# Kernel optimization log

Hardware: AMD Instinct MI355X
Metric: run time of the kernel (lower is better)

The kernel has to match this reference:

```python
import jax, jax.numpy as jnp
import numpy as np

M = 256
N = 256
J = 2
L = 4
F = J * L  # number of Morlet wavelets
PI = float(np.pi)


def _make_grid(m, n):
    gm = np.arange(-(m // 2), -(m // 2) + m, dtype=np.float32)
    gn = np.arange(-(n // 2), -(n // 2) + n, dtype=np.float32)
    return jnp.asarray(np.stack(np.meshgrid(gm, gn, indexing='ij'), 0))  # [2, M, N]

GRID = _make_grid(M, N)


def morlet_filters(theta, xis, sigmas, slants, morlet=True):
    """Build Fourier-domain Morlet (or Gabor/Gaussian) filters, [F, M, N] complex64."""
    c, s = jnp.cos(theta), jnp.sin(theta)
    wave_vectors = jnp.stack([c, s], axis=1) * xis[:, None]                   # [F, 2]
    # orthonormal basis per filter: row0 along wave direction, row1 perpendicular
    basis = jnp.stack([jnp.stack([c, s], 1), jnp.stack([-s, c], 1)], axis=1)  # [F, 2, 2]
    gauss_dirs = basis / sigmas[:, None, None]
    slant_mod = jnp.stack([slants, jnp.ones_like(slants)], axis=1)            # [F, 2]
    gauss_dirs = gauss_dirs * slant_mod[:, :, None]
    phase = jnp.einsum('fd,dmn->fmn', wave_vectors, GRID)                     # [F, M, N]
    waves = jnp.exp(1j * phase)
    radii2 = jnp.sum(jnp.einsum('fed,dmn->femn', gauss_dirs, GRID) ** 2, axis=1)
    gauss = jnp.exp(-0.5 * radii2)
    if morlet:
        gs = gauss.sum(axis=(-2, -1), keepdims=True)
        ws = (waves * gauss).sum(axis=(-2, -1), keepdims=True)
        filt = (waves - ws / gs) * gauss  # zero-mean Morlet correction
    else:
        filt = waves * gauss
    norm = (2.0 * PI * sigmas * sigmas / slants)[:, None, None]
    filt = filt / norm
    filt = jnp.fft.ifftshift(filt, axes=(-2, -1))
    return jnp.fft.fft2(filt)


def low_pass_phi():
    # Gaussian low-pass at scale 2**J (xi = 0, Gabor without Morlet correction)
    th = jnp.zeros((1,), jnp.float32)
    xi = jnp.zeros((1,), jnp.float32)
    sg = jnp.full((1,), 0.8 * 2.0 ** J, jnp.float32)
    sl = jnp.ones((1,), jnp.float32)
    return morlet_filters(th, xi, sg, sl, morlet=False)[0]  # [M, N]


def setup_inputs() -> dict:
    key = jax.random.key(0)
    x = jax.random.normal(key, (4, 2, M, N), dtype=jnp.float32)
    # Tight-Frame initialization of the J*L learnable wavelet parameters
    js = np.repeat(np.arange(J), L).astype(np.float32)
    theta = np.tile((int(L - L / 2 - 1) - np.arange(L)) * np.pi / L, J).astype(np.float32)
    xis = (3.0 / 4.0 * np.pi / 2.0 ** js).astype(np.float32)
    sigmas = (0.8 * 2.0 ** js).astype(np.float32)
    slants = np.full(J * L, 4.0 / L, dtype=np.float32)
    return {"x": x, "theta": jnp.asarray(theta), "xis": jnp.asarray(xis),
            "sigmas": jnp.asarray(sigmas), "slants": jnp.asarray(slants)}


def reference(x, theta, xis, sigmas, slants):
    """Order-2 wavelet scattering on periodic fields via FFT conv + modulus.
    Returns [B, (1 + F + F*F) * C, M, N]."""
    B, C = x.shape[0], x.shape[1]
    sub = 1  # subsample factor (module default)
    psi = morlet_filters(theta, xis, sigmas, slants)        # [F, M, N] complex
    phi = low_pass_phi()                                    # [M, N] complex
    Xh = jnp.fft.fft2(x)                                    # [B, C, M, N]
    S0 = jnp.fft.ifft2(Xh * phi).real[:, :, None]           # [B, C, 1, M, N]
    U1 = jnp.abs(jnp.fft.ifft2(Xh[:, :, None] * psi))       # [B, C, F, M, N]
    U1h = jnp.fft.fft2(U1)
    U2 = jnp.abs(jnp.fft.ifft2(U1h[:, :, :, None] * psi))   # [B, C, F, F, M, N]
    S = jnp.concatenate([S0, U1, U2.reshape(B, C, F * F, M, N)], axis=2)
    S = S[..., ::sub, ::sub]
    return S.reshape(B, (1 + F + F * F) * C, M // sub, N // sub)
```

## Files before the change

kernel.cpp:

```cpp
#include <hip/hip_runtime.h>
#include <math.h>

#define PI_F 3.14159265358979323846f
#define IMG 65536

__device__ __forceinline__ float2 cmul(float2 a, float2 b) {
  return make_float2(a.x * b.x - a.y * b.y, a.x * b.y + a.y * b.x);
}
__device__ __forceinline__ float2 shflx(float2 v, int m) {
  return make_float2(__shfl_xor(v.x, m, 64), __shfl_xor(v.y, m, 64));
}


__device__ __forceinline__ void fft64_dif(float2 v[4], int lane) {
  #pragma unroll
  for (int st = 5; st >= 0; --st) {
    int s = 1 << st;
    float ang = -PI_F * (float)(lane & (s - 1)) / (float)s;
    float sn, cs; __sincosf(ang, &sn, &cs);
    bool hi = (lane & s) != 0;
    #pragma unroll
    for (int r = 0; r < 4; ++r) {
      float2 p = shflx(v[r], s);
      if (hi) {
        float2 d = make_float2(p.x - v[r].x, p.y - v[r].y);
        v[r] = make_float2(d.x * cs - d.y * sn, d.x * sn + d.y * cs);
      } else {
        v[r] = make_float2(v[r].x + p.x, v[r].y + p.y);
      }
    }
  }
}

__device__ __forceinline__ void fft64_dit(float2 v[4], int lane) {
  #pragma unroll
  for (int st = 0; st <= 5; ++st) {
    int s = 1 << st;
    float ang = PI_F * (float)(lane & (s - 1)) / (float)s;
    float sn, cs; __sincosf(ang, &sn, &cs);
    bool hi = (lane & s) != 0;
    #pragma unroll
    for (int r = 0; r < 4; ++r) {
      float2 p = shflx(v[r], s);
      if (hi) {
        float2 wb = make_float2(v[r].x * cs - v[r].y * sn, v[r].x * sn + v[r].y * cs);
        v[r] = make_float2(p.x - wb.x, p.y - wb.y);
      } else {
        float2 wb = make_float2(p.x * cs - p.y * sn, p.x * sn + p.y * cs);
        v[r] = make_float2(v[r].x + wb.x, v[r].y + wb.y);
      }
    }
  }
}

__device__ __forceinline__ void fwd256(float2 v[4], int lane) {
  float2 e0 = make_float2(v[0].x + v[2].x, v[0].y + v[2].y);
  float2 o0 = make_float2(v[0].x - v[2].x, v[0].y - v[2].y);
  float2 e1 = make_float2(v[1].x + v[3].x, v[1].y + v[3].y);
  float2 o1 = make_float2(v[1].x - v[3].x, v[1].y - v[3].y);
  v[0] = make_float2(e0.x + e1.x, e0.y + e1.y);
  v[2] = make_float2(e0.x - e1.x, e0.y - e1.y);
  v[1] = make_float2(o0.x + o1.y, o0.y - o1.x);
  v[3] = make_float2(o0.x - o1.y, o0.y + o1.x);
  float sn, cs; __sincosf(2.f * PI_F * (float)lane * (1.f / 256.f), &sn, &cs);
  float2 w1 = make_float2(cs, -sn);
  float2 w2 = cmul(w1, w1);
  float2 w3 = cmul(w2, w1);
  v[1] = cmul(v[1], w1); v[2] = cmul(v[2], w2); v[3] = cmul(v[3], w3);
  fft64_dif(v, lane);
}

__device__ __forceinline__ void inv256(float2 v[4], int lane) {
  fft64_dit(v, lane);
  float sn, cs; __sincosf(2.f * PI_F * (float)lane * (1.f / 256.f), &sn, &cs);
  float2 w1 = make_float2(cs, sn);
  float2 w2 = cmul(w1, w1);
  float2 w3 = cmul(w2, w1);
  v[1] = cmul(v[1], w1); v[2] = cmul(v[2], w2); v[3] = cmul(v[3], w3);
  float2 e0 = make_float2(v[0].x + v[2].x, v[0].y + v[2].y);
  float2 o0 = make_float2(v[0].x - v[2].x, v[0].y - v[2].y);
  float2 e1 = make_float2(v[1].x + v[3].x, v[1].y + v[3].y);
  float2 o1 = make_float2(v[1].x - v[3].x, v[1].y - v[3].y);
  v[0] = make_float2(e0.x + e1.x, e0.y + e1.y);
  v[2] = make_float2(e0.x - e1.x, e0.y - e1.y);
  v[1] = make_float2(o0.x - o1.y, o0.y + o1.x);
  v[3] = make_float2(o0.x + o1.y, o0.y - o1.x);
}

__device__ __forceinline__ void tile_flush(float2 (*tile)[258], float2* OT, int r0) {
  __syncthreads();
  int t = threadIdx.x;
  float4* dst = (float4*)(OT + (size_t)t * 256 + r0);
  #pragma unroll
  for (int k = 0; k < 4; ++k) {
    float2 a = tile[2 * k][t], b = tile[2 * k + 1][t];
    dst[k] = make_float4(a.x, a.y, b.x, b.y);
  }
}


__global__ __launch_bounds__(256) void k_sums(const float* th, const float* xi,
                                              const float* sg, const float* sl,
                                              float* sums) {
  int f = blockIdx.x, t = threadIdx.x;
  float c, s;
  sincosf(th[f], &s, &c);
  float X = xi[f], S = sg[f], SL = sl[f];
  float a0x = SL * c / S, a0y = SL * s / S, a1x = -s / S, a1y = c / S;
  float gs = 0.f, wr = 0.f, wi = 0.f;
  for (int p = t; p < IMG; p += 256) {
    float gm = (float)((p >> 8) - 128);
    float gn = (float)((p & 255) - 128);
    float r0 = a0x * gm + a0y * gn, r1 = a1x * gm + a1y * gn;
    float g = __expf(-0.5f * (r0 * r0 + r1 * r1));
    float sp, cp;
    sincosf(X * (c * gm + s * gn), &sp, &cp);
    gs += g; wr += cp * g; wi += sp * g;
  }
  __shared__ float red[3][256];
  red[0][t] = gs; red[1][t] = wr; red[2][t] = wi;
  __syncthreads();
  for (int o = 128; o > 0; o >>= 1) {
    if (t < o) {
      red[0][t] += red[0][t + o];
      red[1][t] += red[1][t + o];
      red[2][t] += red[2][t + o];
    }
    __syncthreads();
  }
  if (t == 0) {
    sums[f * 3 + 0] = red[0][0];
    sums[f * 3 + 1] = red[1][0];
    sums[f * 3 + 2] = red[2][0];
  }
}

__global__ __launch_bounds__(256) void k_spatial(const float* th, const float* xi,
                                                 const float* sg, const float* sl,
                                                 const float* sums, float2* spat) {
  int f = blockIdx.y;
  int p = blockIdx.x * 256 + threadIdx.x;
  int m = p >> 8, n = p & 255;
  float gm = (m < 128) ? (float)m : (float)(m - 256);
  float gn = (n < 128) ? (float)n : (float)(n - 256);
  bool isPhi = (f == 8);
  float T = isPhi ? 0.f : th[f];
  float X = isPhi ? 0.f : xi[f];
  float S = isPhi ? 3.2f : sg[f];
  float SL = isPhi ? 1.f : sl[f];
  float c, s;
  sincosf(T, &s, &c);
  float a0x = SL * c / S, a0y = SL * s / S, a1x = -s / S, a1y = c / S;
  float r0 = a0x * gm + a0y * gn, r1 = a1x * gm + a1y * gn;
  float g = __expf(-0.5f * (r0 * r0 + r1 * r1));
  float sp, cp;
  sincosf(X * (c * gm + s * gn), &sp, &cp);
  float re, im;
  if (!isPhi) {
    float gs = sums[f * 3];
    float Kr = sums[f * 3 + 1] / gs, Ki = sums[f * 3 + 2] / gs;
    re = (cp - Kr) * g;
    im = (sp - Ki) * g;
  } else {
    re = g;
    im = 0.f;
  }
  float inorm = SL / (2.f * PI_F * S * S);
  spat[(size_t)f * IMG + p] = make_float2(re * inorm, im * inorm);
}


__global__ __launch_bounds__(256) void k_fwdT(const float2* __restrict__ in,
                                              float2* __restrict__ out) {
  __shared__ float2 tile[8][258];
  int w = threadIdx.x >> 6, l = threadIdx.x & 63;
  int img = blockIdx.y, r0 = blockIdx.x * 8;
  const float2* ib = in + (size_t)img * IMG;
  #pragma unroll
  for (int it = 0; it < 2; ++it) {
    int ri = w + 4 * it;
    const float2* ip = ib + (size_t)(r0 + ri) * 256;
    float2 v[4];
    #pragma unroll
    for (int j = 0; j < 4; ++j) v[j] = ip[l + 64 * j];
    fwd256(v, l);
    #pragma unroll
    for (int j = 0; j < 4; ++j) tile[ri][l + 64 * j] = v[j];
  }
  tile_flush(tile, out + (size_t)img * IMG, r0);
}

__global__ __launch_bounds__(256) void k_fwdT_real(const float* __restrict__ in,
                                                   float2* __restrict__ out) {
  __shared__ float2 tile[8][258];
  int w = threadIdx.x >> 6, l = threadIdx.x & 63;
  int img = blockIdx.y, r0 = blockIdx.x * 8;
  const float* ib = in + (size_t)img * IMG;
  #pragma unroll
  for (int it = 0; it < 2; ++it) {
    int ri = w + 4 * it;
    const float* ip = ib + (size_t)(r0 + ri) * 256;
    float2 v[4];
    #pragma unroll
    for (int j = 0; j < 4; ++j) v[j] = make_float2(ip[l + 64 * j], 0.f);
    fwd256(v, l);
    #pragma unroll
    for (int j = 0; j < 4; ++j) tile[ri][l + 64 * j] = v[j];
  }
  tile_flush(tile, out + (size_t)img * IMG, r0);
}

__global__ __launch_bounds__(256) void k_fwdS(const float2* in, float2* out) {
  int w = threadIdx.x >> 6, l = threadIdx.x & 63;
  int img = blockIdx.y, row = blockIdx.x * 4 + w;
  const float2* ip = in + (size_t)img * IMG + (size_t)row * 256;
  float2 v[4];
  #pragma unroll
  for (int j = 0; j < 4; ++j) v[j] = ip[l + 64 * j];
  fwd256(v, l);
  float2* op = out + (size_t)img * IMG + (size_t)row * 256;
  #pragma unroll
  for (int j = 0; j < 4; ++j) op[l + 64 * j] = v[j];
}

__device__ __forceinline__ void mul_inv_tile(const float2* A, const float2* P,
                                             float2* OT, int r0, int w, int l,
                                             float2 (*tile)[258]) {
  #pragma unroll
  for (int it = 0; it < 2; ++it) {
    int ri = w + 4 * it;
    const float2* ap = A + (size_t)(r0 + ri) * 256;
    const float2* pp = P + (size_t)(r0 + ri) * 256;
    float2 v[4];
    #pragma unroll
    for (int j = 0; j < 4; ++j) v[j] = cmul(ap[l + 64 * j], pp[l + 64 * j]);
    inv256(v, l);
    #pragma unroll
    for (int j = 0; j < 4; ++j) tile[ri][l + 64 * j] = v[j];
  }
  tile_flush(tile, OT, r0);
}

__global__ __launch_bounds__(256) void k_s0_p1(const float2* __restrict__ XhT,
                                               const float2* __restrict__ phiT,
                                               float2* __restrict__ s0t) {
  __shared__ float2 tile[8][258];
  int w = threadIdx.x >> 6, l = threadIdx.x & 63;
  int img = blockIdx.y, r0 = blockIdx.x * 8;
  mul_inv_tile(XhT + (size_t)img * IMG, phiT, s0t + (size_t)img * IMG, r0, w, l, tile);
}

__global__ __launch_bounds__(256) void k_s0_p2(const float2* __restrict__ s0t,
                                               float* __restrict__ out) {
  int w = threadIdx.x >> 6, l = threadIdx.x & 63;
  int img = blockIdx.y, row = blockIdx.x * 4 + w;
  const float2* ip = s0t + (size_t)img * IMG + (size_t)row * 256;
  float2 v[4];
  #pragma unroll
  for (int j = 0; j < 4; ++j) v[j] = ip[l + 64 * j];
  inv256(v, l);
  float* op = out + ((size_t)img * 73) * IMG + (size_t)row * 256;
  #pragma unroll
  for (int j = 0; j < 4; ++j) op[l + 64 * j] = v[j].x * (1.f / 65536.f);
}

__global__ __launch_bounds__(256) void k_u1_p1(const float2* __restrict__ XhT,
                                               const float2* __restrict__ psiT,
                                               float* out) {
  __shared__ float2 tile[8][258];
  int w = threadIdx.x >> 6, l = threadIdx.x & 63;
  int u = blockIdx.y, i = u >> 3, f = u & 7;
  int r0 = blockIdx.x * 8;
  float2* t1 = (float2*)out + ((size_t)(i * 73 + 9 + 2 * f)) * 32768;
  mul_inv_tile(XhT + (size_t)i * IMG, psiT + (size_t)f * IMG, t1, r0, w, l, tile);
}

__global__ __launch_bounds__(256) void k_u1_p2(float* out, float2* T2) {
  __shared__ float2 tile[8][258];
  int w = threadIdx.x >> 6, l = threadIdx.x & 63;
  int u = blockIdx.y, i = u >> 3, f = u & 7;
  int r0 = blockIdx.x * 8;
  const float2* t1 = (const float2*)out + ((size_t)(i * 73 + 9 + 2 * f)) * 32768;
  float* uo = out + ((size_t)(i * 73 + 1 + f)) * IMG;
  #pragma unroll
  for (int it = 0; it < 2; ++it) {
    int ri = w + 4 * it, row = r0 + ri;
    const float2* ip = t1 + (size_t)row * 256;
    float2 v[4];
    #pragma unroll
    for (int j = 0; j < 4; ++j) v[j] = ip[l + 64 * j];
    inv256(v, l);
    float* up = uo + (size_t)row * 256;
    #pragma unroll
    for (int j = 0; j < 4; ++j) {
      float2 z = v[j];
      float mod = sqrtf(z.x * z.x + z.y * z.y) * (1.f / 65536.f);
      up[l + 64 * j] = mod;
      v[j] = make_float2(mod, 0.f);
    }
    fwd256(v, l);
    #pragma unroll
    for (int j = 0; j < 4; ++j) tile[ri][l + 64 * j] = v[j];
  }
  tile_flush(tile, T2 + (size_t)u * IMG, r0);
}

__global__ __launch_bounds__(256) void k_u2_p1(const float2* __restrict__ U1hT,
                                               const float2* __restrict__ psiT,
                                               float2* __restrict__ T3,
                                               int f1, int i0) {
  __shared__ float2 tile[8][258];
  int w = threadIdx.x >> 6, l = threadIdx.x & 63;
  int y = blockIdx.y, ii = i0 + (y >> 3), f2 = y & 7;
  int r0 = blockIdx.x * 8;
  mul_inv_tile(U1hT + ((size_t)(ii * 8 + f1)) * IMG, psiT + (size_t)f2 * IMG,
               T3 + (size_t)y * IMG, r0, w, l, tile);
}

__global__ __launch_bounds__(256) void k_u2_p2(const float2* __restrict__ T3,
                                               float* __restrict__ out,
                                               int f1, int i0) {
  int w = threadIdx.x >> 6, l = threadIdx.x & 63;
  int y = blockIdx.y, ii = i0 + (y >> 3), f2 = y & 7;
  int row = blockIdx.x * 4 + w;
  const float2* ip = T3 + (size_t)y * IMG + (size_t)row * 256;
  float2 v[4];
  #pragma unroll
  for (int j = 0; j < 4; ++j) v[j] = ip[l + 64 * j];
  inv256(v, l);
  float* op = out + ((size_t)(ii * 73 + 9 + f1 * 8 + f2)) * IMG + (size_t)row * 256;
  #pragma unroll
  for (int j = 0; j < 4; ++j) {
    float2 z = v[j];
    op[l + 64 * j] = sqrtf(z.x * z.x + z.y * z.y) * (1.f / 65536.f);
  }
}

extern "C" void kernel_launch(void* const* d_in, const int* in_sizes, int n_in,
                              void* d_out, int out_size, void* d_ws, size_t ws_size,
                              hipStream_t stream) {
  const float* x  = (const float*)d_in[0];
  const float* th = (const float*)d_in[1];
  const float* xi = (const float*)d_in[2];
  const float* sg = (const float*)d_in[3];
  const float* sl = (const float*)d_in[4];
  float* out = (float*)d_out;

  float* sums  = (float*)d_ws;
  float2* psiT = (float2*)((char*)d_ws + 1024);
  float2* XhT  = psiT + (size_t)9 * IMG;
  float2* T2   = XhT + (size_t)8 * IMG;
  float2* T3   = T2 + (size_t)64 * IMG;
  float2* spat = T2;
  float2* tmp9 = T2 + (size_t)9 * IMG;
  float2* xtmp = T2;
  float2* s0t  = T2;

  size_t t3off = 1024 + (size_t)(9 + 8 + 64) * IMG * sizeof(float2);
  int nI = 8;
  while (nI > 1 && t3off + (size_t)nI * 8 * IMG * sizeof(float2) > ws_size) nI >>= 1;

  dim3 B(256);
  k_sums<<<dim3(8), B, 0, stream>>>(th, xi, sg, sl, sums);
  k_spatial<<<dim3(256, 9), B, 0, stream>>>(th, xi, sg, sl, sums, spat);
  k_fwdT<<<dim3(32, 9), B, 0, stream>>>(spat, tmp9);
  k_fwdS<<<dim3(64, 9), B, 0, stream>>>(tmp9, psiT);
  k_fwdT_real<<<dim3(32, 8), B, 0, stream>>>(x, xtmp);
  k_fwdS<<<dim3(64, 8), B, 0, stream>>>(xtmp, XhT);
  k_s0_p1<<<dim3(32, 8), B, 0, stream>>>(XhT, psiT + (size_t)8 * IMG, s0t);
  k_s0_p2<<<dim3(64, 8), B, 0, stream>>>(s0t, out);
  k_u1_p1<<<dim3(32, 64), B, 0, stream>>>(XhT, psiT, out);
  k_u1_p2<<<dim3(32, 64), B, 0, stream>>>(out, T2);
  k_fwdS<<<dim3(64, 64), B, 0, stream>>>(T2, T2);
  for (int f1 = 0; f1 < 8; ++f1)
    for (int i0 = 0; i0 < 8; i0 += nI) {
      k_u2_p1<<<dim3(32, nI * 8), B, 0, stream>>>(T2, psiT, T3, f1, i0);
      k_u2_p2<<<dim3(64, nI * 8), B, 0, stream>>>(T3, out, f1, i0);
    }
}
```

Baseline: 581.1 us.

## Batch eight rows per wave in register FFTs with precomputed twiddles and fewer launches

Each wave now transforms 8 rows held in registers and writes the transpose straight to global memory with float4 stores, dropping the shared-memory tile and its barrier. Twiddles are computed once per lane in a struct and reused across all rows and both passes, replacing per-stage sincos calls. The spatial filter build is fused into the first FFT pass, S0 is folded into the U1 kernels as a ninth filter, and the U2 loop is batched into larger chunks so far fewer kernels are launched. The cost is much higher register pressure from 32 complex values per lane plus twiddles, which may lower occupancy, and the transposed stores are strided across columns.

Result: faster. 539.5 us (-7.2%).

```diff
diff --git a/kernel.cpp b/kernel.cpp
--- a/kernel.cpp
+++ b/kernel.cpp
@@ -11,90 +11,133 @@
   return make_float2(__shfl_xor(v.x, m, 64), __shfl_xor(v.y, m, 64));
 }
 
-
-__device__ __forceinline__ void fft64_dif(float2 v[4], int lane) {
-  #pragma unroll
-  for (int st = 5; st >= 0; --st) {
-    int s = 1 << st;
-    float ang = -PI_F * (float)(lane & (s - 1)) / (float)s;
-    float sn, cs; __sincosf(ang, &sn, &cs);
-    bool hi = (lane & s) != 0;
-    #pragma unroll
-    for (int r = 0; r < 4; ++r) {
-      float2 p = shflx(v[r], s);
-      if (hi) {
-        float2 d = make_float2(p.x - v[r].x, p.y - v[r].y);
-        v[r] = make_float2(d.x * cs - d.y * sn, d.x * sn + d.y * cs);
-      } else {
-        v[r] = make_float2(v[r].x + p.x, v[r].y + p.y);
+struct Tw { float2 w[5]; float2 q1, q2, q3; };
+
+__device__ __forceinline__ void tw_make(int lane, float sign, Tw& T) {
+  #pragma unroll
+  for (int t = 0; t < 5; ++t) {
+    int s = 32 >> t;
+    if (lane & s) {
+      float ang = sign * PI_F * (float)(lane & (s - 1)) / (float)s;
+      float sn, cs; __sincosf(ang, &sn, &cs);
+      T.w[t] = make_float2(cs, sn);
+    } else {
+      T.w[t] = make_float2(1.f, 0.f);
+    }
+  }
+  float ang = sign * 2.f * PI_F * (float)lane * (1.f / 256.f);
+  float sn, cs; __sincosf(ang, &sn, &cs);
+  T.q1 = make_float2(cs, sn);
+  T.q2 = cmul(T.q1, T.q1);
+  T.q3 = cmul(T.q2, T.q1);
+}
+
+
+__device__ __forceinline__ void fwd256_b(float2 (&v)[8][4], int lane, const Tw& T) {
+  #pragma unroll
+  for (int r = 0; r < 8; ++r) {
+    float2 a = v[r][0], b = v[r][1], c = v[r][2], d = v[r][3];
+    float2 e0 = make_float2(a.x + c.x, a.y + c.y);
+    float2 o0 = make_float2(a.x - c.x, a.y - c.y);
+    float2 e1 = make_float2(b.x + d.x, b.y + d.y);
+    float2 o1 = make_float2(b.x - d.x, b.y - d.y);
+    v[r][0] = make_float2(e0.x + e1.x, e0.y + e1.y);
+    v[r][2] = cmul(make_float2(e0.x - e1.x, e0.y - e1.y), T.q2);
+    v[r][1] = cmul(make_float2(o0.x + o1.y, o0.y - o1.x), T.q1);
+    v[r][3] = cmul(make_float2(o0.x - o1.y, o0.y + o1.x), T.q3);
+  }
+  #pragma unroll
+  for (int t = 0; t < 5; ++t) {
+    int s = 32 >> t;
+    float sg = (lane & s) ? -1.f : 1.f;
+    float2 w = T.w[t];
+    #pragma unroll
+    for (int r = 0; r < 8; ++r)
+      #pragma unroll
+      for (int j = 0; j < 4; ++j) {
+        float2 p = shflx(v[r][j], s);
+        float2 u = make_float2(p.x + sg * v[r][j].x, p.y + sg * v[r][j].y);
+        v[r][j] = cmul(u, w);
       }
-    }
-  }
-}
-
-__device__ __forceinline__ void fft64_dit(float2 v[4], int lane) {
-  #pragma unroll
-  for (int st = 0; st <= 5; ++st) {
-    int s = 1 << st;
-    float ang = PI_F * (float)(lane & (s - 1)) / (float)s;
-    float sn, cs; __sincosf(ang, &sn, &cs);
-    bool hi = (lane & s) != 0;
-    #pragma unroll
-    for (int r = 0; r < 4; ++r) {
-      float2 p = shflx(v[r], s);
-      if (hi) {
-        float2 wb = make_float2(v[r].x * cs - v[r].y * sn, v[r].x * sn + v[r].y * cs);
-        v[r] = make_float2(p.x - wb.x, p.y - wb.y);
-      } else {
-        float2 wb = make_float2(p.x * cs - p.y * sn, p.x * sn + p.y * cs);
-        v[r] = make_float2(v[r].x + wb.x, v[r].y + wb.y);
+  }
+  {
+    float sg = (lane & 1) ? -1.f : 1.f;
+    #pragma unroll
+    for (int r = 0; r < 8; ++r)
+      #pragma unroll
+      for (int j = 0; j < 4; ++j) {
+        float2 p = shflx(v[r][j], 1);
+        v[r][j] = make_float2(p.x + sg * v[r][j].x, p.y + sg * v[r][j].y);
       }
-    }
-  }
-}
-
-__device__ __forceinline__ void fwd256(float2 v[4], int lane) {
-  float2 e0 = make_float2(v[0].x + v[2].x, v[0].y + v[2].y);
-  float2 o0 = make_float2(v[0].x - v[2].x, v[0].y - v[2].y);
-  float2 e1 = make_float2(v[1].x + v[3].x, v[1].y + v[3].y);
-  float2 o1 = make_float2(v[1].x - v[3].x, v[1].y - v[3].y);
-  v[0] = make_float2(e0.x + e1.x, e0.y + e1.y);
-  v[2] = make_float2(e0.x - e1.x, e0.y - e1.y);
-  v[1] = make_float2(o0.x + o1.y, o0.y - o1.x);
-  v[3] = make_float2(o0.x - o1.y, o0.y + o1.x);
-  float sn, cs; __sincosf(2.f * PI_F * (float)lane * (1.f / 256.f), &sn, &cs);
-  float2 w1 = make_float2(cs, -sn);
-  float2 w2 = cmul(w1, w1);
-  float2 w3 = cmul(w2, w1);
-  v[1] = cmul(v[1], w1); v[2] = cmul(v[2], w2); v[3] = cmul(v[3], w3);
-  fft64_dif(v, lane);
-}
-
-__device__ __forceinline__ void inv256(float2 v[4], int lane) {
-  fft64_dit(v, lane);
-  float sn, cs; __sincosf(2.f * PI_F * (float)lane * (1.f / 256.f), &sn, &cs);
-  float2 w1 = make_float2(cs, sn);
-  float2 w2 = cmul(w1, w1);
-  float2 w3 = cmul(w2, w1);
-  v[1] = cmul(v[1], w1); v[2] = cmul(v[2], w2); v[3] = cmul(v[3], w3);
-  float2 e0 = make_float2(v[0].x + v[2].x, v[0].y + v[2].y);
-  float2 o0 = make_float2(v[0].x - v[2].x, v[0].y - v[2].y);
-  float2 e1 = make_float2(v[1].x + v[3].x, v[1].y + v[3].y);
-  float2 o1 = make_float2(v[1].x - v[3].x, v[1].y - v[3].y);
-  v[0] = make_float2(e0.x + e1.x, e0.y + e1.y);
-  v[2] = make_float2(e0.x - e1.x, e0.y - e1.y);
-  v[1] = make_float2(o0.x - o1.y, o0.y + o1.x);
-  v[3] = make_float2(o0.x + o1.y, o0.y - o1.x);
-}
-
-__device__ __forceinline__ void tile_flush(float2 (*tile)[258], float2* OT, int r0) {
-  __syncthreads();
-  int t = threadIdx.x;
-  float4* dst = (float4*)(OT + (size_t)t * 256 + r0);
-  #pragma unroll
-  for (int k = 0; k < 4; ++k) {
-    float2 a = tile[2 * k][t], b = tile[2 * k + 1][t];
-    dst[k] = make_float4(a.x, a.y, b.x, b.y);
+  }
+}
+
+__device__ __forceinline__ void inv256_b(float2 (&v)[8][4], int lane, const Tw& T) {
+  {
+    float sg = (lane & 1) ? -1.f : 1.f;
+    #pragma unroll
+    for (int r = 0; r < 8; ++r)
+      #pragma unroll
+      for (int j = 0; j < 4; ++j) {
+        float2 p = shflx(v[r][j], 1);
+        v[r][j] = make_float2(p.x + sg * v[r][j].x, p.y + sg * v[r][j].y);
+      }
+  }
+  #pragma unroll
+  for (int t = 0; t < 5; ++t) {
+    int s = 2 << t;
+    float sg = (lane & s) ? -1.f : 1.f;
+    float2 w = T.w[4 - t];
+    #pragma unroll
+    for (int r = 0; r < 8; ++r)
+      #pragma unroll
+      for (int j = 0; j < 4; ++j) {
+        float2 z = cmul(v[r][j], w);
+        float2 p = shflx(z, s);
+        v[r][j] = make_float2(p.x + sg * z.x, p.y + sg * z.y);
+      }
+  }
+  #pragma unroll
+  for (int r = 0; r < 8; ++r) {
+    float2 a = v[r][0], b = cmul(v[r][1], T.q1);
+    float2 c = cmul(v[r][2], T.q2), d = cmul(v[r][3], T.q3);
+    float2 e0 = make_float2(a.x + c.x, a.y + c.y);
+    float2 o0 = make_float2(a.x - c.x, a.y - c.y);
+    float2 e1 = make_float2(b.x + d.x, b.y + d.y);
+    float2 o1 = make_float2(b.x - d.x, b.y - d.y);
+    v[r][0] = make_float2(e0.x + e1.x, e0.y + e1.y);
+    v[r][2] = make_float2(e0.x - e1.x, e0.y - e1.y);
+    v[r][1] = make_float2(o0.x - o1.y, o0.y + o1.x);
+    v[r][3] = make_float2(o0.x + o1.y, o0.y - o1.x);
+  }
+}
+
+
+__device__ __forceinline__ void loadRows(const float2* bp, int r0, float2 (&v)[8][4], int l) {
+  #pragma unroll
+  for (int ri = 0; ri < 8; ++ri) {
+    const float2* rp = bp + (size_t)(r0 + ri) * 256 + l;
+    #pragma unroll
+    for (int j = 0; j < 4; ++j) v[ri][j] = rp[64 * j];
+  }
+}
+__device__ __forceinline__ void storeRows(float2* bp, int r0, float2 (&v)[8][4], int l) {
+  #pragma unroll
+  for (int ri = 0; ri < 8; ++ri) {
+    float2* rp = bp + (size_t)(r0 + ri) * 256 + l;
+    #pragma unroll
+    for (int j = 0; j < 4; ++j) rp[64 * j] = v[ri][j];
+  }
+}
+__device__ __forceinline__ void storeT(float2* OT, int r0, float2 (&v)[8][4], int l) {
+  #pragma unroll
+  for (int j = 0; j < 4; ++j) {
+    int c = l + 64 * j;
+    float4* dst = (float4*)(OT + (size_t)c * 256 + r0);
+    #pragma unroll
+    for (int k = 0; k < 4; ++k)
+      dst[k] = make_float4(v[2 * k][j].x, v[2 * k][j].y,
+                           v[2 * k + 1][j].x, v[2 * k + 1][j].y);
   }
 }
 
@@ -135,205 +178,167 @@
   }
 }
 
-__global__ __launch_bounds__(256) void k_spatial(const float* th, const float* xi,
-                                                 const float* sg, const float* sl,
-                                                 const float* sums, float2* spat) {
+__global__ __launch_bounds__(256) void k_psi_p1(const float* th, const float* xi,
+                                                const float* sg_, const float* sl,
+                                                const float* sums, float2* outT) {
+  int w = threadIdx.x >> 6, l = threadIdx.x & 63;
   int f = blockIdx.y;
-  int p = blockIdx.x * 256 + threadIdx.x;
-  int m = p >> 8, n = p & 255;
-  float gm = (m < 128) ? (float)m : (float)(m - 256);
-  float gn = (n < 128) ? (float)n : (float)(n - 256);
+  int r0 = blockIdx.x * 32 + w * 8;
   bool isPhi = (f == 8);
-  float T = isPhi ? 0.f : th[f];
-  float X = isPhi ? 0.f : xi[f];
-  float S = isPhi ? 3.2f : sg[f];
-  float SL = isPhi ? 1.f : sl[f];
+  float T_ = 0.f, X = 0.f, S = 3.2f, SL = 1.f, Kr = 0.f, Ki = 0.f;
+  if (!isPhi) {
+    T_ = th[f]; X = xi[f]; S = sg_[f]; SL = sl[f];
+    float gs = sums[f * 3];
+    Kr = sums[f * 3 + 1] / gs;
+    Ki = sums[f * 3 + 2] / gs;
+  }
   float c, s;
-  sincosf(T, &s, &c);
+  sincosf(T_, &s, &c);
   float a0x = SL * c / S, a0y = SL * s / S, a1x = -s / S, a1y = c / S;
-  float r0 = a0x * gm + a0y * gn, r1 = a1x * gm + a1y * gn;
-  float g = __expf(-0.5f * (r0 * r0 + r1 * r1));
-  float sp, cp;
-  sincosf(X * (c * gm + s * gn), &sp, &cp);
-  float re, im;
-  if (!isPhi) {
-    float gs = sums[f * 3];
-    float Kr = sums[f * 3 + 1] / gs, Ki = sums[f * 3 + 2] / gs;
-    re = (cp - Kr) * g;
-    im = (sp - Ki) * g;
-  } else {
-    re = g;
-    im = 0.f;
-  }
   float inorm = SL / (2.f * PI_F * S * S);
-  spat[(size_t)f * IMG + p] = make_float2(re * inorm, im * inorm);
-}
-
-
-__global__ __launch_bounds__(256) void k_fwdT(const float2* __restrict__ in,
-                                              float2* __restrict__ out) {
-  __shared__ float2 tile[8][258];
-  int w = threadIdx.x >> 6, l = threadIdx.x & 63;
-  int img = blockIdx.y, r0 = blockIdx.x * 8;
-  const float2* ib = in + (size_t)img * IMG;
-  #pragma unroll
-  for (int it = 0; it < 2; ++it) {
-    int ri = w + 4 * it;
-    const float2* ip = ib + (size_t)(r0 + ri) * 256;
-    float2 v[4];
-    #pragma unroll
-    for (int j = 0; j < 4; ++j) v[j] = ip[l + 64 * j];
-    fwd256(v, l);
-    #pragma unroll
-    for (int j = 0; j < 4; ++j) tile[ri][l + 64 * j] = v[j];
-  }
-  tile_flush(tile, out + (size_t)img * IMG, r0);
-}
-
-__global__ __launch_bounds__(256) void k_fwdT_real(const float* __restrict__ in,
-                                                   float2* __restrict__ out) {
-  __shared__ float2 tile[8][258];
-  int w = threadIdx.x >> 6, l = threadIdx.x & 63;
-  int img = blockIdx.y, r0 = blockIdx.x * 8;
-  const float* ib = in + (size_t)img * IMG;
-  #pragma unroll
-  for (int it = 0; it < 2; ++it) {
-    int ri = w + 4 * it;
-    const float* ip = ib + (size_t)(r0 + ri) * 256;
-    float2 v[4];
-    #pragma unroll
-    for (int j = 0; j < 4; ++j) v[j] = make_float2(ip[l + 64 * j], 0.f);
-    fwd256(v, l);
-    #pragma unroll
-    for (int j = 0; j < 4; ++j) tile[ri][l + 64 * j] = v[j];
-  }
-  tile_flush(tile, out + (size_t)img * IMG, r0);
+  float2 v[8][4];
+  #pragma unroll
+  for (int ri = 0; ri < 8; ++ri) {
+    int m = r0 + ri;
+    float gm = (m < 128) ? (float)m : (float)(m - 256);
+    #pragma unroll
+    for (int j = 0; j < 4; ++j) {
+      int n = l + 64 * j;
+      float gn = (n < 128) ? (float)n : (float)(n - 256);
+      float rr0 = a0x * gm + a0y * gn, rr1 = a1x * gm + a1y * gn;
+      float g = __expf(-0.5f * (rr0 * rr0 + rr1 * rr1));
+      float sp, cp;
+      sincosf(X * (c * gm + s * gn), &sp, &cp);
+      float re = isPhi ? g : (cp - Kr) * g;
+      float im = isPhi ? 0.f : (sp - Ki) * g;
+      v[ri][j] = make_float2(re * inorm, im * inorm);
+    }
+  }
+  Tw T; tw_make(l, -1.f, T);
+  fwd256_b(v, l, T);
+  storeT(outT + (size_t)f * IMG, r0, v, l);
+}
+
+__global__ __launch_bounds__(256) void k_x_p1(const float* __restrict__ x,
+                                              float2* __restrict__ outT) {
+  int w = threadIdx.x >> 6, l = threadIdx.x & 63;
+  int img = blockIdx.y, r0 = blockIdx.x * 32 + w * 8;
+  float2 v[8][4];
+  #pragma unroll
+  for (int ri = 0; ri < 8; ++ri) {
+    const float* rp = x + (size_t)img * IMG + (size_t)(r0 + ri) * 256 + l;
+    #pragma unroll
+    for (int j = 0; j < 4; ++j) v[ri][j] = make_float2(rp[64 * j], 0.f);
+  }
+  Tw T; tw_make(l, -1.f, T);
+  fwd256_b(v, l, T);
+  storeT(outT + (size_t)img * IMG, r0, v, l);
 }
 
 __global__ __launch_bounds__(256) void k_fwdS(const float2* in, float2* out) {
   int w = threadIdx.x >> 6, l = threadIdx.x & 63;
-  int img = blockIdx.y, row = blockIdx.x * 4 + w;
-  const float2* ip = in + (size_t)img * IMG + (size_t)row * 256;
-  float2 v[4];
-  #pragma unroll
-  for (int j = 0; j < 4; ++j) v[j] = ip[l + 64 * j];
-  fwd256(v, l);
-  float2* op = out + (size_t)img * IMG + (size_t)row * 256;
-  #pragma unroll
-  for (int j = 0; j < 4; ++j) op[l + 64 * j] = v[j];
-}
-
-__device__ __forceinline__ void mul_inv_tile(const float2* A, const float2* P,
-                                             float2* OT, int r0, int w, int l,
-                                             float2 (*tile)[258]) {
-  #pragma unroll
-  for (int it = 0; it < 2; ++it) {
-    int ri = w + 4 * it;
-    const float2* ap = A + (size_t)(r0 + ri) * 256;
-    const float2* pp = P + (size_t)(r0 + ri) * 256;
-    float2 v[4];
-    #pragma unroll
-    for (int j = 0; j < 4; ++j) v[j] = cmul(ap[l + 64 * j], pp[l + 64 * j]);
-    inv256(v, l);
-    #pragma unroll
-    for (int j = 0; j < 4; ++j) tile[ri][l + 64 * j] = v[j];
-  }
-  tile_flush(tile, OT, r0);
-}
-
-__global__ __launch_bounds__(256) void k_s0_p1(const float2* __restrict__ XhT,
-                                               const float2* __restrict__ phiT,
-                                               float2* __restrict__ s0t) {
-  __shared__ float2 tile[8][258];
-  int w = threadIdx.x >> 6, l = threadIdx.x & 63;
-  int img = blockIdx.y, r0 = blockIdx.x * 8;
-  mul_inv_tile(XhT + (size_t)img * IMG, phiT, s0t + (size_t)img * IMG, r0, w, l, tile);
-}
-
-__global__ __launch_bounds__(256) void k_s0_p2(const float2* __restrict__ s0t,
-                                               float* __restrict__ out) {
-  int w = threadIdx.x >> 6, l = threadIdx.x & 63;
-  int img = blockIdx.y, row = blockIdx.x * 4 + w;
-  const float2* ip = s0t + (size_t)img * IMG + (size_t)row * 256;
-  float2 v[4];
-  #pragma unroll
-  for (int j = 0; j < 4; ++j) v[j] = ip[l + 64 * j];
-  inv256(v, l);
-  float* op = out + ((size_t)img * 73) * IMG + (size_t)row * 256;
-  #pragma unroll
-  for (int j = 0; j < 4; ++j) op[l + 64 * j] = v[j].x * (1.f / 65536.f);
+  int img = blockIdx.y, r0 = blockIdx.x * 32 + w * 8;
+  float2 v[8][4];
+  loadRows(in + (size_t)img * IMG, r0, v, l);
+  Tw T; tw_make(l, -1.f, T);
+  fwd256_b(v, l, T);
+  storeRows(out + (size_t)img * IMG, r0, v, l);
 }
 
 __global__ __launch_bounds__(256) void k_u1_p1(const float2* __restrict__ XhT,
                                                const float2* __restrict__ psiT,
                                                float* out) {
-  __shared__ float2 tile[8][258];
-  int w = threadIdx.x >> 6, l = threadIdx.x & 63;
-  int u = blockIdx.y, i = u >> 3, f = u & 7;
-  int r0 = blockIdx.x * 8;
-  float2* t1 = (float2*)out + ((size_t)(i * 73 + 9 + 2 * f)) * 32768;
-  mul_inv_tile(XhT + (size_t)i * IMG, psiT + (size_t)f * IMG, t1, r0, w, l, tile);
+  int w = threadIdx.x >> 6, l = threadIdx.x & 63;
+  int y = blockIdx.y, i = y / 9, f = y - i * 9;
+  int r0 = blockIdx.x * 32 + w * 8;
+  const float2* A = XhT + (size_t)i * IMG;
+  const float2* P = psiT + (size_t)f * IMG;
+  float2 v[8][4];
+  #pragma unroll
+  for (int ri = 0; ri < 8; ++ri) {
+    const float2* ap = A + (size_t)(r0 + ri) * 256 + l;
+    const float2* pp = P + (size_t)(r0 + ri) * 256 + l;
+    #pragma unroll
+    for (int j = 0; j < 4; ++j) v[ri][j] = cmul(ap[64 * j], pp[64 * j]);
+  }
+  Tw T; tw_make(l, 1.f, T);
+  inv256_b(v, l, T);
+  storeT((float2*)out + ((size_t)(i * 73 + 9 + 2 * f)) * 32768, r0, v, l);
 }
 
 __global__ __launch_bounds__(256) void k_u1_p2(float* out, float2* T2) {
-  __shared__ float2 tile[8][258];
-  int w = threadIdx.x >> 6, l = threadIdx.x & 63;
-  int u = blockIdx.y, i = u >> 3, f = u & 7;
-  int r0 = blockIdx.x * 8;
-  const float2* t1 = (const float2*)out + ((size_t)(i * 73 + 9 + 2 * f)) * 32768;
-  float* uo = out + ((size_t)(i * 73 + 1 + f)) * IMG;
-  #pragma unroll
-  for (int it = 0; it < 2; ++it) {
-    int ri = w + 4 * it, row = r0 + ri;
-    const float2* ip = t1 + (size_t)row * 256;
-    float2 v[4];
-    #pragma unroll
-    for (int j = 0; j < 4; ++j) v[j] = ip[l + 64 * j];
-    inv256(v, l);
-    float* up = uo + (size_t)row * 256;
+  int w = threadIdx.x >> 6, l = threadIdx.x & 63;
+  int y = blockIdx.y, i = y / 9, f = y - i * 9;
+  int r0 = blockIdx.x * 32 + w * 8;
+  float2 v[8][4];
+  loadRows((const float2*)out + ((size_t)(i * 73 + 9 + 2 * f)) * 32768, r0, v, l);
+  Tw Ti; tw_make(l, 1.f, Ti);
+  inv256_b(v, l, Ti);
+  if (f == 8) {
+    float* op = out + (size_t)(i * 73) * IMG;
+    #pragma unroll
+    for (int ri = 0; ri < 8; ++ri)
+      #pragma unroll
+      for (int j = 0; j < 4; ++j)
+        op[(size_t)(r0 + ri) * 256 + l + 64 * j] = v[ri][j].x * (1.f / 65536.f);
+    return;
+  }
+  float* uo = out + (size_t)(i * 73 + 1 + f) * IMG;
+  #pragma unroll
+  for (int ri = 0; ri < 8; ++ri)
     #pragma unroll
     for (int j = 0; j < 4; ++j) {
-      float2 z = v[j];
+      float2 z = v[ri][j];
       float mod = sqrtf(z.x * z.x + z.y * z.y) * (1.f / 65536.f);
-      up[l + 64 * j] = mod;
-      v[j] = make_float2(mod, 0.f);
-    }
-    fwd256(v, l);
-    #pragma unroll
-    for (int j = 0; j < 4; ++j) tile[ri][l + 64 * j] = v[j];
-  }
-  tile_flush(tile, T2 + (size_t)u * IMG, r0);
+      uo[(size_t)(r0 + ri) * 256 + l + 64 * j] = mod;
+      v[ri][j] = make_float2(mod, 0.f);
+    }
+  Tw Tf; tw_make(l, -1.f, Tf);
+  fwd256_b(v, l, Tf);
+  storeT(T2 + (size_t)(i * 8 + f) * IMG, r0, v, l);
 }
 
 __global__ __launch_bounds__(256) void k_u2_p1(const float2* __restrict__ U1hT,
                                                const float2* __restrict__ psiT,
-                                               float2* __restrict__ T3,
-                                               int f1, int i0) {
-  __shared__ float2 tile[8][258];
-  int w = threadIdx.x >> 6, l = threadIdx.x & 63;
-  int y = blockIdx.y, ii = i0 + (y >> 3), f2 = y & 7;
-  int r0 = blockIdx.x * 8;
-  mul_inv_tile(U1hT + ((size_t)(ii * 8 + f1)) * IMG, psiT + (size_t)f2 * IMG,
-               T3 + (size_t)y * IMG, r0, w, l, tile);
+                                               float2* __restrict__ T3, int q0) {
+  int w = threadIdx.x >> 6, l = threadIdx.x & 63;
+  int y = blockIdx.y, q = q0 + (y >> 3), f2 = y & 7;
+  int f1 = q >> 3, ii = q & 7;
+  int r0 = blockIdx.x * 32 + w * 8;
+  const float2* A = U1hT + (size_t)(ii * 8 + f1) * IMG;
+  const float2* P = psiT + (size_t)f2 * IMG;
+  float2 v[8][4];
+  #pragma unroll
+  for (int ri = 0; ri < 8; ++ri) {
+    const float2* ap = A + (size_t)(r0 + ri) * 256 + l;
+    const float2* pp = P + (size_t)(r0 + ri) * 256 + l;
+    #pragma unroll
+    for (int j = 0; j < 4; ++j) v[ri][j] = cmul(ap[64 * j], pp[64 * j]);
+  }
+  Tw T; tw_make(l, 1.f, T);
+  inv256_b(v, l, T);
+  storeT(T3 + (size_t)y * IMG, r0, v, l);
 }
 
 __global__ __launch_bounds__(256) void k_u2_p2(const float2* __restrict__ T3,
-                                               float* __restrict__ out,
-                                               int f1, int i0) {
-  int w = threadIdx.x >> 6, l = threadIdx.x & 63;
-  int y = blockIdx.y, ii = i0 + (y >> 3), f2 = y & 7;
-  int row = blockIdx.x * 4 + w;
-  const float2* ip = T3 + (size_t)y * IMG + (size_t)row * 256;
-  float2 v[4];
-  #pragma unroll
-  for (int j = 0; j < 4; ++j) v[j] = ip[l + 64 * j];
-  inv256(v, l);
-  float* op = out + ((size_t)(ii * 73 + 9 + f1 * 8 + f2)) * IMG + (size_t)row * 256;
-  #pragma unroll
-  for (int j = 0; j < 4; ++j) {
-    float2 z = v[j];
-    op[l + 64 * j] = sqrtf(z.x * z.x + z.y * z.y) * (1.f / 65536.f);
-  }
+                                               float* __restrict__ out, int q0) {
+  int w = threadIdx.x >> 6, l = threadIdx.x & 63;
+  int y = blockIdx.y, q = q0 + (y >> 3), f2 = y & 7;
+  int f1 = q >> 3, ii = q & 7;
+  int r0 = blockIdx.x * 32 + w * 8;
+  float2 v[8][4];
+  loadRows(T3 + (size_t)y * IMG, r0, v, l);
+  Tw T; tw_make(l, 1.f, T);
+  inv256_b(v, l, T);
+  float* op = out + (size_t)(ii * 73 + 9 + f1 * 8 + f2) * IMG;
+  #pragma unroll
+  for (int ri = 0; ri < 8; ++ri)
+    #pragma unroll
+    for (int j = 0; j < 4; ++j) {
+      float2 z = v[ri][j];
+      op[(size_t)(r0 + ri) * 256 + l + 64 * j] =
+          sqrtf(z.x * z.x + z.y * z.y) * (1.f / 65536.f);
+    }
 }
 
 extern "C" void kernel_launch(void* const* d_in, const int* in_sizes, int n_in,
@@ -351,30 +356,24 @@
   float2* XhT  = psiT + (size_t)9 * IMG;
   float2* T2   = XhT + (size_t)8 * IMG;
   float2* T3   = T2 + (size_t)64 * IMG;
-  float2* spat = T2;
-  float2* tmp9 = T2 + (size_t)9 * IMG;
+  float2* tmp9 = T2;
   float2* xtmp = T2;
-  float2* s0t  = T2;
-
-  size_t t3off = 1024 + (size_t)(9 + 8 + 64) * IMG * sizeof(float2);
-  int nI = 8;
-  while (nI > 1 && t3off + (size_t)nI * 8 * IMG * sizeof(float2) > ws_size) nI >>= 1;
+
+  size_t base = 1024 + (size_t)(9 + 8 + 64) * IMG * sizeof(float2);
+  int CQ = 64;
+  while (CQ > 1 && base + (size_t)CQ * 8 * IMG * sizeof(float2) > ws_size) CQ >>= 1;
 
   dim3 B(256);
-  k_sums<<<dim3(8), B, 0, stream>>>(th, xi, sg, sl, sums);
-  k_spatial<<<dim3(256, 9), B, 0, stream>>>(th, xi, sg, sl, sums, spat);
-  k_fwdT<<<dim3(32, 9), B, 0, stream>>>(spat, tmp9);
-  k_fwdS<<<dim3(64, 9), B, 0, stream>>>(tmp9, psiT);
-  k_fwdT_real<<<dim3(32, 8), B, 0, stream>>>(x, xtmp);
-  k_fwdS<<<dim3(64, 8), B, 0, stream>>>(xtmp, XhT);
-  k_s0_p1<<<dim3(32, 8), B, 0, stream>>>(XhT, psiT + (size_t)8 * IMG, s0t);
-  k_s0_p2<<<dim3(64, 8), B, 0, stream>>>(s0t, out);
-  k_u1_p1<<<dim3(32, 64), B, 0, stream>>>(XhT, psiT, out);
-  k_u1_p2<<<dim3(32, 64), B, 0, stream>>>(out, T2);
-  k_fwdS<<<dim3(64, 64), B, 0, stream>>>(T2, T2);
-  for (int f1 = 0; f1 < 8; ++f1)
-    for (int i0 = 0; i0 < 8; i0 += nI) {
-      k_u2_p1<<<dim3(32, nI * 8), B, 0, stream>>>(T2, psiT, T3, f1, i0);
-      k_u2_p2<<<dim3(64, nI * 8), B, 0, stream>>>(T3, out, f1, i0);
-    }
-}
+  k_sums  <<<dim3(8),     B, 0, stream>>>(th, xi, sg, sl, sums);
+  k_psi_p1<<<dim3(8, 9),  B, 0, stream>>>(th, xi, sg, sl, sums, tmp9);
+  k_fwdS  <<<dim3(8, 9),  B, 0, stream>>>(tmp9, psiT);
+  k_x_p1  <<<dim3(8, 8),  B, 0, stream>>>(x, xtmp);
+  k_fwdS  <<<dim3(8, 8),  B, 0, stream>>>(xtmp, XhT);
+  k_u1_p1 <<<dim3(8, 72), B, 0, stream>>>(XhT, psiT, out);
+  k_u1_p2 <<<dim3(8, 72), B, 0, stream>>>(out, T2);
+  k_fwdS  <<<dim3(8, 64), B, 0, stream>>>(T2, T2);
+  for (int q0 = 0; q0 < 64; q0 += CQ) {
+    k_u2_p1<<<dim3(8, CQ * 8), B, 0, stream>>>(T2, psiT, T3, q0);
+    k_u2_p2<<<dim3(8, CQ * 8), B, 0, stream>>>(T3, out, q0);
+  }
+}
```
